# Performance work log

Hardware: AMD Instinct MI355X
Metric: run time of the kernel (lower is better)

The kernel has to match this reference:

```python
import jax, jax.numpy as jnp
import numpy as np

ALPHA = 0.2  # LeakyReLU negative slope


def setup_inputs() -> dict:
    key = jax.random.key(0)
    k1, k2, k3, k4 = jax.random.split(key, 4)
    N, IN, OUT = 8192, 512, 256
    x = jax.random.normal(k1, (N, IN), dtype=jnp.float32)
    adj = jnp.zeros((N, N), dtype=jnp.float32)  # accepted but unused by the module
    W = jax.random.normal(k2, (OUT, IN), dtype=jnp.float32) * (1.0 / np.sqrt(IN))
    a1 = jax.random.normal(k3, (OUT,), dtype=jnp.float32) * (1.0 / np.sqrt(OUT))
    a2 = jax.random.normal(k4, (OUT,), dtype=jnp.float32) * (1.0 / np.sqrt(OUT))
    return {"x": x, "adj": adj, "W": W, "a1": a1, "a2": a2}


def reference(x, adj, W, a1, a2):
    # h = tran(x): [N, OUT]
    h = x @ W.T
    # additive GAT scores: e[i, j] = a2 . h_i + a1 . h_j  (from unsqueeze(0)+unsqueeze(1))
    s1 = h @ a1  # [N], att1(h)
    s2 = h @ a2  # [N], att2(h)
    e = s2[:, None] + s1[None, :]  # [N, N]
    e = jnp.where(e > 0, e, ALPHA * e)  # LeakyReLU
    attn = jax.nn.softmax(e, axis=1)  # softmax over dim=1; dropout is identity in eval
    return attn @ h  # [N, OUT]
```

## Files before the change

### kernel.cpp

```cpp
#include <hip/hip_runtime.h>

#define NROW 8192
#define DIN  512
#define DOUT 256
#define NCHUNK 256
#define CLEN 32

constexpr size_t OFF_H      = 0;
constexpr size_t OFF_S1     = OFF_H + (size_t)NROW*DOUT*4;
constexpr size_t OFF_S2     = OFF_S1 + NROW*4;
constexpr size_t OFF_RANK   = OFF_S2 + NROW*4;
constexpr size_t OFF_MISC   = OFF_RANK + NROW*4;
constexpr size_t MEMSET_LEN = OFF_MISC + 256 - OFF_S1;
constexpr size_t OFF_S1S    = OFF_MISC + 256;
constexpr size_t OFF_PERM   = OFF_S1S + NROW*4;
constexpr size_t OFF_WHI    = OFF_PERM + NROW*4;
constexpr size_t OFF_WLO    = OFF_WHI + NROW*4;
constexpr size_t OFF_PRELOS = OFF_WLO + NROW*4;
constexpr size_t OFF_SUFHIS = OFF_PRELOS + 33024;
constexpr size_t OFF_CSLO   = OFF_SUFHIS + 33024;
constexpr size_t OFF_CSHI   = OFF_CSLO + 1024;
constexpr size_t OFF_TLO    = OFF_CSHI + 1024;
constexpr size_t OFF_THI    = OFF_TLO + (size_t)NCHUNK*DOUT*4;
constexpr size_t OFF_PRELO  = OFF_THI + (size_t)NCHUNK*DOUT*4;
constexpr size_t OFF_SUFHI  = OFF_PRELO + (size_t)(NROW+1)*DOUT*4;
constexpr size_t WS_NEED    = OFF_SUFHI + (size_t)(NROW+1)*DOUT*4;

__global__ __launch_bounds__(256) void gemm_h(const float* __restrict__ x,
                                              const float* __restrict__ W,
                                              const float* __restrict__ a1,
                                              const float* __restrict__ a2,
                                              float* __restrict__ h,
                                              float* __restrict__ s1,
                                              float* __restrict__ s2) {
  __shared__ float xs[64][68];
  __shared__ float ws[64][68];
  const int tid = threadIdx.x;
  const int rowBase = blockIdx.x * 64;
  const int colBase = blockIdx.y * 64;
  const int ty = tid >> 4, tx = tid & 15;
  float acc[4][4] = {};
  for (int k0 = 0; k0 < DIN; k0 += 64) {
#pragma unroll
    for (int i = 0; i < 4; ++i) {
      int s = i * 256 + tid;
      int r = s >> 4;
      int kk = (s & 15) << 2;
      float4 v = *(const float4*)(x + (size_t)(rowBase + r) * DIN + k0 + kk);
      xs[kk + 0][r] = v.x; xs[kk + 1][r] = v.y; xs[kk + 2][r] = v.z; xs[kk + 3][r] = v.w;
      float4 u = *(const float4*)(W + (size_t)(colBase + r) * DIN + k0 + kk);
      ws[kk + 0][r] = u.x; ws[kk + 1][r] = u.y; ws[kk + 2][r] = u.z; ws[kk + 3][r] = u.w;
    }
    __syncthreads();
#pragma unroll
    for (int kk = 0; kk < 64; ++kk) {
      float4 av = *(const float4*)&xs[kk][ty << 2];
      float4 bv = *(const float4*)&ws[kk][tx << 2];
      float a[4] = {av.x, av.y, av.z, av.w};
      float b[4] = {bv.x, bv.y, bv.z, bv.w};
#pragma unroll
      for (int r = 0; r < 4; ++r)
#pragma unroll
        for (int c = 0; c < 4; ++c) acc[r][c] = fmaf(a[r], b[c], acc[r][c]);
    }
    __syncthreads();
  }
#pragma unroll
  for (int r = 0; r < 4; ++r) {
    float4 o = make_float4(acc[r][0], acc[r][1], acc[r][2], acc[r][3]);
    *(float4*)(h + (size_t)(rowBase + (ty << 2) + r) * DOUT + colBase + (tx << 2)) = o;
  }
  float4 A1 = *(const float4*)(a1 + colBase + (tx << 2));
  float4 A2 = *(const float4*)(a2 + colBase + (tx << 2));
#pragma unroll
  for (int r = 0; r < 4; ++r) {
    float p1 = acc[r][0] * A1.x + acc[r][1] * A1.y + acc[r][2] * A1.z + acc[r][3] * A1.w;
    float p2 = acc[r][0] * A2.x + acc[r][1] * A2.y + acc[r][2] * A2.z + acc[r][3] * A2.w;
#pragma unroll
    for (int m = 1; m < 16; m <<= 1) {
      p1 += __shfl_xor(p1, m);
      p2 += __shfl_xor(p2, m);
    }
    if (tx == 0) {
      int row = rowBase + (ty << 2) + r;
      atomicAdd(&s1[row], p1);
      atomicAdd(&s2[row], p2);
    }
  }
}

__global__ __launch_bounds__(256) void rank_count(const float* __restrict__ s1,
                                                  int* __restrict__ rank,
                                                  unsigned int* __restrict__ miscu) {
  __shared__ float sj[1024];
  __shared__ float wm[4];
  const int t = threadIdx.x;
  const int ib = blockIdx.x, jc = blockIdx.y;
  const int j0 = jc * 1024;
  *(float4*)&sj[t << 2] = *(const float4*)(s1 + j0 + (t << 2));
  const int i = ib * 256 + t;
  const float v = s1[i];
  __syncthreads();
  int cnt = 0;
#pragma unroll 4
  for (int q = 0; q < 256; ++q) {
    float4 sv = *(const float4*)&sj[q << 2];
    int jg = j0 + (q << 2);
    cnt += (int)(sv.x < v) + (int)((sv.x == v) & (jg + 0 < i));
    cnt += (int)(sv.y < v) + (int)((sv.y == v) & (jg + 1 < i));
    cnt += (int)(sv.z < v) + (int)((sv.z == v) & (jg + 2 < i));
    cnt += (int)(sv.w < v) + (int)((sv.w == v) & (jg + 3 < i));
  }
  atomicAdd(&rank[i], cnt);
  if (jc == 0) {
    float m = v;
#pragma unroll
    for (int off = 32; off > 0; off >>= 1) m = fmaxf(m, __shfl_down(m, off));
    if ((t & 63) == 0) wm[t >> 6] = m;
    __syncthreads();
    if (t == 0) {
      float mm = fmaxf(fmaxf(wm[0], wm[1]), fmaxf(wm[2], wm[3]));
      unsigned int b = __float_as_uint(mm);
      unsigned int enc = (b & 0x80000000u) ? ~b : (b | 0x80000000u);
      atomicMax(miscu, enc);
    }
  }
}

__global__ __launch_bounds__(256) void scatter_w(const float* __restrict__ s1,
                                                 const int* __restrict__ rank,
                                                 const unsigned int* __restrict__ miscu,
                                                 float* __restrict__ miscf,
                                                 float* __restrict__ s1s,
                                                 int* __restrict__ perm,
                                                 float* __restrict__ w_hi,
                                                 float* __restrict__ w_lo) {
  const int i = blockIdx.x * 256 + threadIdx.x;
  unsigned int e = miscu[0];
  unsigned int b = (e & 0x80000000u) ? (e & 0x7fffffffu) : ~e;
  const float M1 = __uint_as_float(b);
  const float v = s1[i];
  const int r = rank[i];
  s1s[r] = v;
  perm[r] = i;
  w_hi[r] = __expf(v - M1);
  w_lo[r] = __expf(0.2f * (v - M1));
  if (i == 0) miscf[0] = M1;
}

__global__ __launch_bounds__(256) void chunk_totals(const float* __restrict__ h,
                                                    const int* __restrict__ perm,
                                                    const float* __restrict__ w_hi,
                                                    const float* __restrict__ w_lo,
                                                    float* __restrict__ T_lo,
                                                    float* __restrict__ T_hi,
                                                    float* __restrict__ cs_lo,
                                                    float* __restrict__ cs_hi) {
  const int d = threadIdx.x, b = blockIdx.x;
  const int j0 = b * CLEN;
  float tlo = 0.f, thi = 0.f;
#pragma unroll
  for (int e = 0; e < CLEN; e += 4) {
    int4 p4 = *(const int4*)(perm + j0 + e);
    float4 wl4 = *(const float4*)(w_lo + j0 + e);
    float4 wh4 = *(const float4*)(w_hi + j0 + e);
    float h0 = h[(size_t)p4.x * DOUT + d];
    float h1 = h[(size_t)p4.y * DOUT + d];
    float h2 = h[(size_t)p4.z * DOUT + d];
    float h3 = h[(size_t)p4.w * DOUT + d];
    tlo += wl4.x * h0 + wl4.y * h1 + wl4.z * h2 + wl4.w * h3;
    thi += wh4.x * h0 + wh4.y * h1 + wh4.z * h2 + wh4.w * h3;
  }
  T_lo[b * DOUT + d] = tlo;
  T_hi[b * DOUT + d] = thi;
  if (d < 64) {
    float wl = (d < 32) ? w_lo[j0 + d] : 0.f;
    float wh = (d < 32) ? w_hi[j0 + d] : 0.f;
#pragma unroll
    for (int off = 32; off > 0; off >>= 1) {
      wl += __shfl_down(wl, off);
      wh += __shfl_down(wh, off);
    }
    if (d == 0) { cs_lo[b] = wl; cs_hi[b] = wh; }
  }
}

__global__ __launch_bounds__(256) void write_prefix(const float* __restrict__ h,
                                                    const int* __restrict__ perm,
                                                    const float* __restrict__ w_hi,
                                                    const float* __restrict__ w_lo,
                                                    const float* __restrict__ T_lo,
                                                    const float* __restrict__ T_hi,
                                                    const float* __restrict__ cs_lo,
                                                    const float* __restrict__ cs_hi,
                                                    float* __restrict__ PreLo,
                                                    float* __restrict__ SufHi,
                                                    float* __restrict__ prelo_s,
                                                    float* __restrict__ sufhi_s) {
  const int d = threadIdx.x, b = blockIdx.x;
  const int j0 = b * CLEN;
  if (d < 64) {
    float accp = 0.f, acct = 0.f;
    for (int p = d; p < NCHUNK; p += 64) {
      float cl = cs_lo[p], ch = cs_hi[p];
      accp += (p < b) ? cl : 0.f;
      acct += (p > b) ? ch : 0.f;
    }
#pragma unroll
    for (int off = 32; off > 0; off >>= 1) {
      accp += __shfl_down(accp, off);
      acct += __shfl_down(acct, off);
    }
    float pres  = __shfl(accp, 0);
    float tails = __shfl(acct, 0);
    float wl = (d < 32) ? w_lo[j0 + d] : 0.f;
    float wh = (d < 32) ? w_hi[j0 + d] : 0.f;
    float pl = wl, ph = wh;
#pragma unroll
    for (int off = 1; off < 32; off <<= 1) {
      float a = __shfl_up(pl, off);
      float c = __shfl_up(ph, off);
      if (d >= off) { pl += a; ph += c; }
    }
    float chunk_hi_tot = __shfl(ph, 31);
    if (d < 32) {
      prelo_s[j0 + d] = pres + (pl - wl);
      sufhi_s[j0 + d] = tails + (chunk_hi_tot - (ph - wh));
    }
    if (b == NCHUNK - 1 && d == 31) {
      prelo_s[NROW] = pres + pl;
      sufhi_s[NROW] = 0.f;
    }
  }
  float rl = 0.f, tail = 0.f;
#pragma unroll 8
  for (int p = 0; p < NCHUNK; ++p) {
    float vl = T_lo[p * DOUT + d];
    float vh = T_hi[p * DOUT + d];
    rl   += (p < b) ? vl : 0.f;
    tail += (p > b) ? vh : 0.f;
  }
  float hv[CLEN], wlv[CLEN], whv[CLEN];
  float ownHi = 0.f;
#pragma unroll
  for (int e = 0; e < CLEN; e += 4) {
    int4 p4 = *(const int4*)(perm + j0 + e);
    float4 wl4 = *(const float4*)(w_lo + j0 + e);
    float4 wh4 = *(const float4*)(w_hi + j0 + e);
    hv[e + 0] = h[(size_t)p4.x * DOUT + d];
    hv[e + 1] = h[(size_t)p4.y * DOUT + d];
    hv[e + 2] = h[(size_t)p4.z * DOUT + d];
    hv[e + 3] = h[(size_t)p4.w * DOUT + d];
    wlv[e + 0] = wl4.x; wlv[e + 1] = wl4.y; wlv[e + 2] = wl4.z; wlv[e + 3] = wl4.w;
    whv[e + 0] = wh4.x; whv[e + 1] = wh4.y; whv[e + 2] = wh4.z; whv[e + 3] = wh4.w;
    ownHi += wh4.x * hv[e] + wh4.y * hv[e + 1] + wh4.z * hv[e + 2] + wh4.w * hv[e + 3];
  }
  float shb = tail + ownHi;
  float preh = 0.f;
#pragma unroll
  for (int e = 0; e < CLEN; ++e) {
    size_t j = (size_t)(j0 + e);
    PreLo[j * DOUT + d] = rl;
    SufHi[j * DOUT + d] = shb - preh;
    rl   += wlv[e] * hv[e];
    preh += whv[e] * hv[e];
  }
  if (b == NCHUNK - 1) {
    PreLo[(size_t)NROW * DOUT + d] = rl;
    SufHi[(size_t)NROW * DOUT + d] = 0.f;
  }
}

__global__ __launch_bounds__(256) void finalize(const float* __restrict__ s2,
                                                const float* __restrict__ s1s,
                                                const float* __restrict__ miscf,
                                                const float* __restrict__ PreLo,
                                                const float* __restrict__ SufHi,
                                                const float* __restrict__ prelo_s,
                                                const float* __restrict__ sufhi_s,
                                                float* __restrict__ out) {
  const int wave = threadIdx.x >> 6, lane = threadIdx.x & 63;
  const int i = blockIdx.x * 4 + wave;
  const float c = s2[i];
  const float M1 = miscf[0];
  const float tval = -c;
  int lo = 0, hi = NROW;
  while (lo < hi) {
    int mid = (lo + hi) >> 1;
    if (s1s[mid] <= tval) lo = mid + 1; else hi = mid;
  }
  const int k = lo;
  const float u = c + M1;
  const float m = fmaxf(u, 0.2f * u);
  const float fh = __expf(u - m);
  const float fl = __expf(0.2f * u - m);
  const float den = fh * sufhi_s[k] + fl * prelo_s[k];
  const float inv = 1.f / den;
  float4 A = *(const float4*)(SufHi + (size_t)k * DOUT + (lane << 2));
  float4 B = *(const float4*)(PreLo + (size_t)k * DOUT + (lane << 2));
  float4 o;
  o.x = (fh * A.x + fl * B.x) * inv;
  o.y = (fh * A.y + fl * B.y) * inv;
  o.z = (fh * A.z + fl * B.z) * inv;
  o.w = (fh * A.w + fl * B.w) * inv;
  *(float4*)(out + (size_t)i * DOUT + (lane << 2)) = o;
}

extern "C" void kernel_launch(void* const* d_in, const int* in_sizes, int n_in,
                              void* d_out, int out_size, void* d_ws, size_t ws_size,
                              hipStream_t stream) {
  const float* x  = (const float*)d_in[0];
  const float* W  = (const float*)d_in[2];
  const float* a1 = (const float*)d_in[3];
  const float* a2 = (const float*)d_in[4];
  float* out = (float*)d_out;

  char* ws = (char*)d_ws;
  if (ws_size < WS_NEED) ws = (char*)d_in[1];

  float*        h       = (float*)(ws + OFF_H);
  float*        s1      = (float*)(ws + OFF_S1);
  float*        s2      = (float*)(ws + OFF_S2);
  int*          rank    = (int*)  (ws + OFF_RANK);
  unsigned int* miscu   = (unsigned int*)(ws + OFF_MISC);
  float*        miscf   = (float*)(ws + OFF_MISC) + 1;
  float*        s1s     = (float*)(ws + OFF_S1S);
  int*          perm    = (int*)  (ws + OFF_PERM);
  float*        w_hi    = (float*)(ws + OFF_WHI);
  float*        w_lo    = (float*)(ws + OFF_WLO);
  float*        prelo_s = (float*)(ws + OFF_PRELOS);
  float*        sufhi_s = (float*)(ws + OFF_SUFHIS);
  float*        cs_lo   = (float*)(ws + OFF_CSLO);
  float*        cs_hi   = (float*)(ws + OFF_CSHI);
  float*        T_lo    = (float*)(ws + OFF_TLO);
  float*        T_hi    = (float*)(ws + OFF_THI);
  float*        PreLo   = (float*)(ws + OFF_PRELO);
  float*        SufHi   = (float*)(ws + OFF_SUFHI);

  hipMemsetAsync(s1, 0, MEMSET_LEN, stream);

  gemm_h<<<dim3(NROW / 64, DOUT / 64), 256, 0, stream>>>(x, W, a1, a2, h, s1, s2);
  rank_count<<<dim3(NROW / 256, 8), 256, 0, stream>>>(s1, rank, miscu);
  scatter_w<<<NROW / 256, 256, 0, stream>>>(s1, rank, miscu, miscf, s1s, perm, w_hi, w_lo);
  chunk_totals<<<NCHUNK, 256, 0, stream>>>(h, perm, w_hi, w_lo, T_lo, T_hi, cs_lo, cs_hi);
  write_prefix<<<NCHUNK, 256, 0, stream>>>(h, perm, w_hi, w_lo, T_lo, T_hi, cs_lo, cs_hi,
                                           PreLo, SufHi, prelo_s, sufhi_s);
  finalize<<<NROW / 4, 256, 0, stream>>>(s2, s1s, miscf, PreLo, SufHi, prelo_s, sufhi_s, out);
}
```

Measured before the change: 402.8 us.

## Replace atomics with per-tile partial scores and fuse rank and scatter kernels

The GEMM now writes per-column-block partial attention scores instead of atomically accumulating them, which removes the memset and the atomics. The rank count and the scatter are merged into one kernel that sums the partials into shared memory, ranks each row with 8 threads plus shuffle reduction, and writes the permutation directly. The max-subtraction stabilisation (M1) is dropped, and the finalize step now uses plain exp(c) and exp(0.2c). That removes two launches and a global max reduction, but it risks overflow if the scores are large. Each block now redundantly sums all 8192 partial scores into shared memory.

```diff
diff --git a/kernel.cpp b/kernel.cpp
--- a/kernel.cpp
+++ b/kernel.cpp
@@ -7,20 +7,17 @@
 #define CLEN 32
 
 constexpr size_t OFF_H      = 0;
-constexpr size_t OFF_S1     = OFF_H + (size_t)NROW*DOUT*4;
-constexpr size_t OFF_S2     = OFF_S1 + NROW*4;
-constexpr size_t OFF_RANK   = OFF_S2 + NROW*4;
-constexpr size_t OFF_MISC   = OFF_RANK + NROW*4;
-constexpr size_t MEMSET_LEN = OFF_MISC + 256 - OFF_S1;
-constexpr size_t OFF_S1S    = OFF_MISC + 256;
+constexpr size_t OFF_S1P    = OFF_H + (size_t)NROW*DOUT*4;
+constexpr size_t OFF_S2P    = OFF_S1P + (size_t)4*NROW*4;
+constexpr size_t OFF_S1S    = OFF_S2P + (size_t)4*NROW*4;
 constexpr size_t OFF_PERM   = OFF_S1S + NROW*4;
 constexpr size_t OFF_WHI    = OFF_PERM + NROW*4;
 constexpr size_t OFF_WLO    = OFF_WHI + NROW*4;
 constexpr size_t OFF_PRELOS = OFF_WLO + NROW*4;
 constexpr size_t OFF_SUFHIS = OFF_PRELOS + 33024;
 constexpr size_t OFF_CSLO   = OFF_SUFHIS + 33024;
-constexpr size_t OFF_CSHI   = OFF_CSLO + 1024;
-constexpr size_t OFF_TLO    = OFF_CSHI + 1024;
+constexpr size_t OFF_CSHI   = OFF_CSLO + (size_t)NCHUNK*4;
+constexpr size_t OFF_TLO    = OFF_CSHI + (size_t)NCHUNK*4;
 constexpr size_t OFF_THI    = OFF_TLO + (size_t)NCHUNK*DOUT*4;
 constexpr size_t OFF_PRELO  = OFF_THI + (size_t)NCHUNK*DOUT*4;
 constexpr size_t OFF_SUFHI  = OFF_PRELO + (size_t)(NROW+1)*DOUT*4;
@@ -31,8 +28,8 @@
                                               const float* __restrict__ a1,
                                               const float* __restrict__ a2,
                                               float* __restrict__ h,
-                                              float* __restrict__ s1,
-                                              float* __restrict__ s2) {
+                                              float* __restrict__ s1p,
+                                              float* __restrict__ s2p) {
   __shared__ float xs[64][68];
   __shared__ float ws[64][68];
   const int tid = threadIdx.x;
@@ -72,6 +69,7 @@
   }
   float4 A1 = *(const float4*)(a1 + colBase + (tx << 2));
   float4 A2 = *(const float4*)(a2 + colBase + (tx << 2));
+  const int cb = colBase >> 6;
 #pragma unroll
   for (int r = 0; r < 4; ++r) {
     float p1 = acc[r][0] * A1.x + acc[r][1] * A1.y + acc[r][2] * A1.z + acc[r][3] * A1.w;
@@ -83,69 +81,58 @@
     }
     if (tx == 0) {
       int row = rowBase + (ty << 2) + r;
-      atomicAdd(&s1[row], p1);
-      atomicAdd(&s2[row], p2);
-    }
-  }
-}
-
-__global__ __launch_bounds__(256) void rank_count(const float* __restrict__ s1,
-                                                  int* __restrict__ rank,
-                                                  unsigned int* __restrict__ miscu) {
-  __shared__ float sj[1024];
-  __shared__ float wm[4];
-  const int t = threadIdx.x;
-  const int ib = blockIdx.x, jc = blockIdx.y;
+      s1p[cb * NROW + row] = p1;
+      s2p[cb * NROW + row] = p2;
+    }
+  }
+}
+
+__global__ __launch_bounds__(256) void ranksc(const float* __restrict__ s1p,
+                                              float* __restrict__ s1s,
+                                              int* __restrict__ perm,
+                                              float* __restrict__ w_hi,
+                                              float* __restrict__ w_lo) {
+  __shared__ float sj[NROW];
+  const int t = threadIdx.x, b = blockIdx.x;
+  const float4* p0 = (const float4*)s1p;
+  const float4* p1 = (const float4*)(s1p + NROW);
+  const float4* p2 = (const float4*)(s1p + 2 * NROW);
+  const float4* p3 = (const float4*)(s1p + 3 * NROW);
+#pragma unroll
+  for (int u = t; u < NROW / 4; u += 256) {
+    float4 a = p0[u], c = p1[u], e = p2[u], f = p3[u];
+    float4 s;
+    s.x = a.x + c.x + e.x + f.x;
+    s.y = a.y + c.y + e.y + f.y;
+    s.z = a.z + c.z + e.z + f.z;
+    s.w = a.w + c.w + e.w + f.w;
+    *(float4*)&sj[u << 2] = s;
+  }
+  __syncthreads();
+  const int rloc = t >> 3, jc = t & 7;
+  const int i = b * 32 + rloc;
+  const float v1 = sj[i];
   const int j0 = jc * 1024;
-  *(float4*)&sj[t << 2] = *(const float4*)(s1 + j0 + (t << 2));
-  const int i = ib * 256 + t;
-  const float v = s1[i];
-  __syncthreads();
   int cnt = 0;
 #pragma unroll 4
-  for (int q = 0; q < 256; ++q) {
-    float4 sv = *(const float4*)&sj[q << 2];
+  for (int qq = 0; qq < 256; ++qq) {
+    int q = (qq + jc) & 255;
     int jg = j0 + (q << 2);
-    cnt += (int)(sv.x < v) + (int)((sv.x == v) & (jg + 0 < i));
-    cnt += (int)(sv.y < v) + (int)((sv.y == v) & (jg + 1 < i));
-    cnt += (int)(sv.z < v) + (int)((sv.z == v) & (jg + 2 < i));
-    cnt += (int)(sv.w < v) + (int)((sv.w == v) & (jg + 3 < i));
-  }
-  atomicAdd(&rank[i], cnt);
+    float4 sv = *(const float4*)&sj[jg];
+    cnt += (int)(sv.x < v1) + (int)((sv.x == v1) & (jg + 0 < i));
+    cnt += (int)(sv.y < v1) + (int)((sv.y == v1) & (jg + 1 < i));
+    cnt += (int)(sv.z < v1) + (int)((sv.z == v1) & (jg + 2 < i));
+    cnt += (int)(sv.w < v1) + (int)((sv.w == v1) & (jg + 3 < i));
+  }
+  cnt += __shfl_xor(cnt, 1);
+  cnt += __shfl_xor(cnt, 2);
+  cnt += __shfl_xor(cnt, 4);
   if (jc == 0) {
-    float m = v;
-#pragma unroll
-    for (int off = 32; off > 0; off >>= 1) m = fmaxf(m, __shfl_down(m, off));
-    if ((t & 63) == 0) wm[t >> 6] = m;
-    __syncthreads();
-    if (t == 0) {
-      float mm = fmaxf(fmaxf(wm[0], wm[1]), fmaxf(wm[2], wm[3]));
-      unsigned int b = __float_as_uint(mm);
-      unsigned int enc = (b & 0x80000000u) ? ~b : (b | 0x80000000u);
-      atomicMax(miscu, enc);
-    }
-  }
-}
-
-__global__ __launch_bounds__(256) void scatter_w(const float* __restrict__ s1,
-                                                 const int* __restrict__ rank,
-                                                 const unsigned int* __restrict__ miscu,
-                                                 float* __restrict__ miscf,
-                                                 float* __restrict__ s1s,
-                                                 int* __restrict__ perm,
-                                                 float* __restrict__ w_hi,
-                                                 float* __restrict__ w_lo) {
-  const int i = blockIdx.x * 256 + threadIdx.x;
-  unsigned int e = miscu[0];
-  unsigned int b = (e & 0x80000000u) ? (e & 0x7fffffffu) : ~e;
-  const float M1 = __uint_as_float(b);
-  const float v = s1[i];
-  const int r = rank[i];
-  s1s[r] = v;
-  perm[r] = i;
-  w_hi[r] = __expf(v - M1);
-  w_lo[r] = __expf(0.2f * (v - M1));
-  if (i == 0) miscf[0] = M1;
+    perm[cnt] = i;
+    s1s[cnt] = v1;
+    w_hi[cnt] = __expf(v1);
+    w_lo[cnt] = __expf(0.2f * v1);
+  }
 }
 
 __global__ __launch_bounds__(256) void chunk_totals(const float* __restrict__ h,
@@ -271,9 +258,8 @@
   }
 }
 
-__global__ __launch_bounds__(256) void finalize(const float* __restrict__ s2,
+__global__ __launch_bounds__(256) void finalize(const float* __restrict__ s2p,
                                                 const float* __restrict__ s1s,
-                                                const float* __restrict__ miscf,
                                                 const float* __restrict__ PreLo,
                                                 const float* __restrict__ SufHi,
                                                 const float* __restrict__ prelo_s,
@@ -281,8 +267,7 @@
                                                 float* __restrict__ out) {
   const int wave = threadIdx.x >> 6, lane = threadIdx.x & 63;
   const int i = blockIdx.x * 4 + wave;
-  const float c = s2[i];
-  const float M1 = miscf[0];
+  const float c = s2p[i] + s2p[NROW + i] + s2p[2 * NROW + i] + s2p[3 * NROW + i];
   const float tval = -c;
   int lo = 0, hi = NROW;
   while (lo < hi) {
@@ -290,10 +275,8 @@
     if (s1s[mid] <= tval) lo = mid + 1; else hi = mid;
   }
   const int k = lo;
-  const float u = c + M1;
-  const float m = fmaxf(u, 0.2f * u);
-  const float fh = __expf(u - m);
-  const float fl = __expf(0.2f * u - m);
+  const float fh = __expf(c);
+  const float fl = __expf(0.2f * c);
   const float den = fh * sufhi_s[k] + fl * prelo_s[k];
   const float inv = 1.f / den;
   float4 A = *(const float4*)(SufHi + (size_t)k * DOUT + (lane << 2));
@@ -318,32 +301,26 @@
   char* ws = (char*)d_ws;
   if (ws_size < WS_NEED) ws = (char*)d_in[1];
 
-  float*        h       = (float*)(ws + OFF_H);
-  float*        s1      = (float*)(ws + OFF_S1);
-  float*        s2      = (float*)(ws + OFF_S2);
-  int*          rank    = (int*)  (ws + OFF_RANK);
-  unsigned int* miscu   = (unsigned int*)(ws + OFF_MISC);
-  float*        miscf   = (float*)(ws + OFF_MISC) + 1;
-  float*        s1s     = (float*)(ws + OFF_S1S);
-  int*          perm    = (int*)  (ws + OFF_PERM);
-  float*        w_hi    = (float*)(ws + OFF_WHI);
-  float*        w_lo    = (float*)(ws + OFF_WLO);
-  float*        prelo_s = (float*)(ws + OFF_PRELOS);
-  float*        sufhi_s = (float*)(ws + OFF_SUFHIS);
-  float*        cs_lo   = (float*)(ws + OFF_CSLO);
-  float*        cs_hi   = (float*)(ws + OFF_CSHI);
-  float*        T_lo    = (float*)(ws + OFF_TLO);
-  float*        T_hi    = (float*)(ws + OFF_THI);
-  float*        PreLo   = (float*)(ws + OFF_PRELO);
-  float*        SufHi   = (float*)(ws + OFF_SUFHI);
-
-  hipMemsetAsync(s1, 0, MEMSET_LEN, stream);
-
-  gemm_h<<<dim3(NROW / 64, DOUT / 64), 256, 0, stream>>>(x, W, a1, a2, h, s1, s2);
-  rank_count<<<dim3(NROW / 256, 8), 256, 0, stream>>>(s1, rank, miscu);
-  scatter_w<<<NROW / 256, 256, 0, stream>>>(s1, rank, miscu, miscf, s1s, perm, w_hi, w_lo);
+  float* h       = (float*)(ws + OFF_H);
+  float* s1p     = (float*)(ws + OFF_S1P);
+  float* s2p     = (float*)(ws + OFF_S2P);
+  float* s1s     = (float*)(ws + OFF_S1S);
+  int*   perm    = (int*)  (ws + OFF_PERM);
+  float* w_hi    = (float*)(ws + OFF_WHI);
+  float* w_lo    = (float*)(ws + OFF_WLO);
+  float* prelo_s = (float*)(ws + OFF_PRELOS);
+  float* sufhi_s = (float*)(ws + OFF_SUFHIS);
+  float* cs_lo   = (float*)(ws + OFF_CSLO);
+  float* cs_hi   = (float*)(ws + OFF_CSHI);
+  float* T_lo    = (float*)(ws + OFF_TLO);
+  float* T_hi    = (float*)(ws + OFF_THI);
+  float* PreLo   = (float*)(ws + OFF_PRELO);
+  float* SufHi   = (float*)(ws + OFF_SUFHI);
+
+  gemm_h<<<dim3(NROW / 64, DOUT / 64), 256, 0, stream>>>(x, W, a1, a2, h, s1p, s2p);
+  ranksc<<<NROW / 32, 256, 0, stream>>>(s1p, s1s, perm, w_hi, w_lo);
   chunk_totals<<<NCHUNK, 256, 0, stream>>>(h, perm, w_hi, w_lo, T_lo, T_hi, cs_lo, cs_hi);
   write_prefix<<<NCHUNK, 256, 0, stream>>>(h, perm, w_hi, w_lo, T_lo, T_hi, cs_lo, cs_hi,
                                            PreLo, SufHi, prelo_s, sufhi_s);
-  finalize<<<NROW / 4, 256, 0, stream>>>(s2, s1s, miscf, PreLo, SufHi, prelo_s, sufhi_s, out);
-}
+  finalize<<<NROW / 4, 256, 0, stream>>>(s2p, s1s, PreLo, SufHi, prelo_s, sufhi_s, out);
+}
```

Result: slower. 446.2 us (+10.8%).
